# Kernel optimization log

Measured on AMD Instinct MI355X. Metric: run time of the kernel, lower is better.

The kernel has to match this reference:

```python
import jax, jax.numpy as jnp
import numpy as np

B, N, E, D = 4, 4096, 2048, 128
MAX_L = 10


def setup_inputs() -> dict:
    key = jax.random.key(0)
    ks = jax.random.split(key, 8)
    x = jax.random.normal(ks[0], (B, N, D), dtype=jnp.float32)
    incidence = jax.random.uniform(ks[1], (B, N, E), dtype=jnp.float32)
    edge_orders = jax.random.randint(ks[2], (B, E), 0, MAX_L + 1)
    # positive normalizer to avoid division blow-up
    prefix_normalizer = jax.random.uniform(ks[3], (B, E), dtype=jnp.float32) + 0.5
    node_mask = jnp.ones((B, N), dtype=bool)
    edge_mask = jnp.ones((B, E), dtype=bool)
    n_nodes = jnp.full((B,), float(N), dtype=jnp.float32)
    # learned tables: Positional2DWeight(2, max_l+1, D, D) and PositionalWeight(max_l+1, 1, D)
    w_table = jax.random.normal(ks[4], (2, MAX_L + 1, D, D), dtype=jnp.float32) * (1.0 / np.sqrt(D))
    b_table = jax.random.normal(ks[5], (MAX_L + 1, D), dtype=jnp.float32) * 0.02
    return {"x": x, "incidence": incidence, "edge_orders": edge_orders,
            "prefix_normalizer": prefix_normalizer, "node_mask": node_mask,
            "edge_mask": edge_mask, "n_nodes": n_nodes,
            "w_table": w_table, "b_table": b_table}


def reference(x, incidence, edge_orders, prefix_normalizer, node_mask, edge_mask,
              n_nodes, w_table, b_table):
    # mask invalid nodes
    x = jnp.where(node_mask[..., None], x, 0.0)  # [B,N,D]
    # per-edge weight gather (the duplicated [B,E,D,D] tensors)
    w0 = w_table[0][edge_orders]  # [B,E,D,D]
    w1 = w_table[1][edge_orders]  # [B,E,D,D]
    w0_1 = w_table[0, 1]          # [D,D]
    w1_1 = w_table[1, 1]          # [D,D]
    # global mean pooling over nodes
    x0 = jnp.sum(x, axis=1, keepdims=True) / n_nodes[:, None, None]  # [B,1,D]
    # incidence-based V2E aggregation
    x1_e = jnp.einsum('bne,bnd->bed', incidence, x) / prefix_normalizer[..., None]
    x1_e = jnp.where(edge_mask[..., None], x1_e, 0.0)  # [B,E,D]
    # node branch: shared order-1 weights
    x_v = jnp.einsum('bnd,do->bno', x0, w0_1) + jnp.einsum('bnd,do->bno', x, w1_1)
    # edge branch: per-edge-order weights
    x_e = jnp.einsum('bd,bedo->beo', x0[:, 0], w0) + jnp.einsum('bed,bedo->beo', x1_e, w1)
    x_v = jnp.where(node_mask[..., None], x_v, 0.0)
    x_e = jnp.where(edge_mask[..., None], x_e, 0.0)
    # BiasE
    bias_e = b_table[edge_orders]            # [B,E,D]
    bias_1 = b_table[1][None, None, :]       # [1,1,D]
    x_v = jnp.where(node_mask[..., None], x_v + bias_1, 0.0)
    x_e = jnp.where(edge_mask[..., None], x_e + bias_e, 0.0)
    return x_v, x_e
```

## Files before the change

### kernel.cpp

```cpp
#include <hip/hip_runtime.h>

#define Bb 4
#define Nn 4096
#define Ee 2048
#define Dd 128
#define NL 11
#define NTMAX 560
#define ZS 4
#define CH 256
#define NP (CH / 2)
#define LDP 132
#define NCHUNK ((Nn / ZS) / CH)
#define NB_EIN (Bb * (Ee / 32) * ZS)
#define NB_XV (Bb * (Nn / 64))

typedef unsigned short u16;
typedef unsigned int u32;
typedef __attribute__((ext_vector_type(8))) short short8;
typedef __attribute__((ext_vector_type(4))) float floatx4;

__device__ __forceinline__ u32 pk2(float lo, float hi) {
    u32 r;
    asm("v_cvt_pk_bf16_f32 %0, %1, %2" : "=v"(r) : "v"(lo), "v"(hi));
    return r;
}
union S8U { u32 u[4]; short8 s; };

__global__ __launch_bounds__(256) void k_prep(const float* __restrict__ x,
                                              const float* __restrict__ wt,
                                              const int* __restrict__ ord,
                                              u32* __restrict__ xt,
                                              float* __restrict__ part,
                                              u32* __restrict__ wt1T,
                                              int* __restrict__ cnt,
                                              int* __restrict__ offs,
                                              int* __restrict__ idx,
                                              int* __restrict__ tilemap) {
    int blk = blockIdx.x, t = threadIdx.x;
    if (blk < 2048) {
        int b = blk & 3, n0b = (blk >> 2) & 127, d0b = blk >> 9;
        int n0 = n0b * 32, d0 = d0b * 32;
        __shared__ float tile[32][33];
        int r = t >> 5, c = t & 31;
#pragma unroll
        for (int i = 0; i < 4; i++)
            tile[r + 8 * i][c] = x[((size_t)b * Nn + n0 + r + 8 * i) * Dd + d0 + c];
        __syncthreads();
#pragma unroll
        for (int i = 0; i < 2; i++) {
            int idx2 = t + 256 * i;
            int dl = idx2 >> 4, cp = idx2 & 15;
            u32 v = pk2(tile[2 * cp][dl], tile[2 * cp + 1][dl]);
            xt[(size_t)(b * Dd + d0 + dl) * (Nn / 2) + (n0 >> 1) + cp] = v;
        }
        if (t < 32) {
            float s = 0.f;
#pragma unroll
            for (int rr = 0; rr < 32; rr++) s += tile[rr][t];
            part[((size_t)(b * 4 + d0b) * 128 + n0b) * 32 + t] = s;
        }
    } else if (blk < 2224) {
        int rr = blk - 2048;
        int l = rr >> 4, sub = rr & 15;
        int d0 = (sub >> 2) * 32, o0 = (sub & 3) * 32;
        __shared__ float tile[32][33];
        const float* w1 = wt + (size_t)(NL + l) * Dd * Dd;
        int r = t >> 5, c = t & 31;
#pragma unroll
        for (int i = 0; i < 4; i++)
            tile[r + 8 * i][c] = w1[(size_t)(d0 + r + 8 * i) * Dd + o0 + c];
        __syncthreads();
#pragma unroll
        for (int i = 0; i < 2; i++) {
            int idx2 = t + 256 * i;
            int ol = idx2 >> 4, dp = idx2 & 15;
            u32 v = pk2(tile[2 * dp][ol], tile[2 * dp + 1][ol]);
            wt1T[(size_t)(l * Dd + o0 + ol) * (Dd / 2) + (d0 >> 1) + dp] = v;
        }
    } else {
        __shared__ int scnt[Bb * NL], soff[Bb * NL], scur[Bb * NL];
        if (t < Bb * NL) { scnt[t] = 0; scur[t] = 0; }
        __syncthreads();
        for (int g = t; g < Bb * Ee; g += 256)
            atomicAdd(&scnt[(g >> 11) * NL + ord[g]], 1);
        __syncthreads();
        if (t == 0) {
            int off = 0, pos = 0;
            for (int i = 0; i < Bb * NL; i++) {
                soff[i] = off;
                offs[i] = off;
                cnt[i] = scnt[i];
                int al = (scnt[i] + 15) & ~15;
                off += al;
                for (int j = 0; j < (al >> 4); j++) tilemap[pos++] = (i << 16) | j;
            }
            for (; pos < NTMAX; pos++) tilemap[pos] = -1;
        }
        for (int i = t; i < 8960; i += 256) idx[i] = 0;
        __syncthreads();
        for (int g = t; g < Bb * Ee; g += 256) {
            int bk = (g >> 11) * NL + ord[g];
            int pos = soff[bk] + atomicAdd(&scur[bk], 1);
            idx[pos] = g & 2047;
        }
    }
}

__global__ __launch_bounds__(128) void k_xe0(const float* __restrict__ part,
                                             const float* __restrict__ wt,
                                             const float* __restrict__ bt,
                                             float* __restrict__ xe0b) {
    int b = blockIdx.x, l = blockIdx.y, o = threadIdx.x;
    __shared__ float ssum[Dd];
    const float* pp = part + ((size_t)(b * 4 + (o >> 5)) * 128) * 32 + (o & 31);
    float s = 0.f;
    for (int nb = 0; nb < 128; nb++) s += pp[nb * 32];
    ssum[o] = s;
    __syncthreads();
    const float* w0 = wt + (size_t)l * Dd * Dd + o;
    float acc = 0.f;
    for (int d = 0; d < Dd; ++d) acc += ssum[d] * w0[(size_t)d * Dd];
    xe0b[(b * NL + l) * Dd + o] = acc * (1.0f / Nn) + bt[l * Dd + o];
}

__global__ __launch_bounds__(256, 4) void k_main(const float* __restrict__ inc,
                                                 const u32* __restrict__ xt,
                                                 const float* __restrict__ x,
                                                 const u32* __restrict__ wt1T,
                                                 const float* __restrict__ xe0b,
                                                 float* __restrict__ x1p,
                                                 float* __restrict__ outv) {
    int blk = blockIdx.x, t = threadIdx.x;
    int w = t >> 6, lane = t & 63, lm = lane & 15, quad = lane >> 4;
    if (blk < NB_EIN) {
        int b = blk & 3, et0 = ((blk >> 2) & 63) * 32, s = blk >> 8;
        int nbase = s * (Nn / ZS);
        __shared__ u32 bufA[2][32][LDP];
        const float* src = inc + ((size_t)b * Nn + nbase) * Ee + et0;
        int pr = t >> 3, c4 = t & 7;

        const u32* bp0 = xt + ((size_t)b * Dd + w * 32 + lm) * (Nn / 2) + (nbase >> 1);
        const u32* bp1 = bp0 + (size_t)16 * (Nn / 2);
        floatx4 a00 = {0.f,0.f,0.f,0.f}, a01 = {0.f,0.f,0.f,0.f};
        floatx4 a10 = {0.f,0.f,0.f,0.f}, a11 = {0.f,0.f,0.f,0.f};

        float4 sA[8], sB[8];
        auto ldchunk = [&](int ci, float4* st) {
#pragma unroll
            for (int j = 0; j < 4; j++) {
                const float* p0 = src + (size_t)(ci * CH + 2 * (pr + 32 * j)) * Ee + 4 * c4;
                st[2 * j]     = *(const float4*)p0;
                st[2 * j + 1] = *(const float4*)(p0 + Ee);
            }
        };
        auto wrchunk = [&](int cb, const float4* st) {
#pragma unroll
            for (int j = 0; j < 4; j++) {
                bufA[cb][4 * c4 + 0][pr + 32 * j] = pk2(st[2 * j].x, st[2 * j + 1].x);
                bufA[cb][4 * c4 + 1][pr + 32 * j] = pk2(st[2 * j].y, st[2 * j + 1].y);
                bufA[cb][4 * c4 + 2][pr + 32 * j] = pk2(st[2 * j].z, st[2 * j + 1].z);
                bufA[cb][4 * c4 + 3][pr + 32 * j] = pk2(st[2 * j].w, st[2 * j + 1].w);
            }
        };
        ldchunk(0, sA);
        ldchunk(1, sB);
        wrchunk(0, sA);
        __syncthreads();

        for (int i = 0; i < NCHUNK; i++) {
            int cb = i & 1;
            if (i + 2 < NCHUNK) { if (cb == 0) ldchunk(i + 2, sA); else ldchunk(i + 2, sB); }
            int ko = i * NP;
#pragma unroll
            for (int ks = 0; ks < 8; ks++) {
                short8 A0 = *(const short8*)&bufA[cb][lm][ks * 16 + quad * 4];
                short8 A1 = *(const short8*)&bufA[cb][16 + lm][ks * 16 + quad * 4];
                short8 B0 = *(const short8*)(bp0 + ko + ks * 16 + quad * 4);
                short8 B1 = *(const short8*)(bp1 + ko + ks * 16 + quad * 4);
                a00 = __builtin_amdgcn_mfma_f32_16x16x32_bf16(A0, B0, a00, 0, 0, 0);
                a01 = __builtin_amdgcn_mfma_f32_16x16x32_bf16(A0, B1, a01, 0, 0, 0);
                a10 = __builtin_amdgcn_mfma_f32_16x16x32_bf16(A1, B0, a10, 0, 0, 0);
                a11 = __builtin_amdgcn_mfma_f32_16x16x32_bf16(A1, B1, a11, 0, 0, 0);
            }
            if (i < NCHUNK - 1) { if (cb == 0) wrchunk(1, sB); else wrchunk(0, sA); }
            __syncthreads();
        }

        int db = w * 32 + lm;
        float* base = x1p + ((size_t)(s * Bb + b) * Ee) * Dd;
#pragma unroll
        for (int r = 0; r < 4; r++) {
            float* q0 = base + (size_t)(et0 + quad * 4 + r) * Dd;
            q0[db] = a00[r];
            q0[db + 16] = a01[r];
            float* q1 = base + (size_t)(et0 + 16 + quad * 4 + r) * Dd;
            q1[db] = a10[r];
            q1[db + 16] = a11[r];
        }
    } else {
        int rr = blk - NB_EIN;
        int b = rr & 3, n0 = (rr >> 2) * 64;
        const float* xrow = x + ((size_t)b * Nn + n0 + w * 16 + lm) * Dd;
        const u32* wrow = wt1T + (size_t)1 * Dd * (Dd / 2);
        floatx4 acc[8];
#pragma unroll
        for (int ot = 0; ot < 8; ot++) acc[ot] = (floatx4){0.f, 0.f, 0.f, 0.f};
#pragma unroll
        for (int ks = 0; ks < 4; ks++) {
            float4 va = *(const float4*)(xrow + ks * 32 + quad * 8);
            float4 vb = *(const float4*)(xrow + ks * 32 + quad * 8 + 4);
            S8U A;
            A.u[0] = pk2(va.x, va.y); A.u[1] = pk2(va.z, va.w);
            A.u[2] = pk2(vb.x, vb.y); A.u[3] = pk2(vb.z, vb.w);
#pragma unroll
            for (int ot = 0; ot < 8; ot++) {
                short8 Bf = *(const short8*)(wrow + (size_t)(ot * 16 + lm) * (Dd / 2) +
                                             ks * 16 + quad * 4);
                acc[ot] = __builtin_amdgcn_mfma_f32_16x16x32_bf16(A.s, Bf, acc[ot], 0, 0, 0);
            }
        }
#pragma unroll
        for (int ot = 0; ot < 8; ot++) {
            float basev = xe0b[(b * NL + 1) * Dd + ot * 16 + lm];
#pragma unroll
            for (int r = 0; r < 4; r++)
                outv[((size_t)b * Nn + n0 + w * 16 + quad * 4 + r) * Dd + ot * 16 + lm] =
                    acc[ot][r] + basev;
        }
    }
}

__global__ __launch_bounds__(256) void k_epi(const float* __restrict__ x1p,
                                             const float* __restrict__ pref,
                                             const u32* __restrict__ wt1T,
                                             const float* __restrict__ xe0b,
                                             const int* __restrict__ cnt,
                                             const int* __restrict__ offs,
                                             const int* __restrict__ idx,
                                             const int* __restrict__ tilemap,
                                             float* __restrict__ oute) {
    int t = threadIdx.x, w = t >> 6, lane = t & 63, lm = lane & 15, quad = lane >> 4;
    int ent = tilemap[blockIdx.x * 4 + w];
    if (ent < 0) return;
    int bk = ent >> 16, j = ent & 0xffff;
    int bb = bk / NL, l = bk % NL;
    int off = offs[bk], cntv = cnt[bk];
    int eA = idx[off + j * 16 + lm];
    float rp = 1.0f / pref[bb * Ee + eA];
    const float* p0 = x1p + ((size_t)bb * Ee + eA) * Dd;
    const u32* wrow = wt1T + (size_t)l * Dd * (Dd / 2);
    floatx4 acc[8];
#pragma unroll
    for (int ot = 0; ot < 8; ot++) acc[ot] = (floatx4){0.f, 0.f, 0.f, 0.f};
#pragma unroll
    for (int ks = 0; ks < 4; ks++) {
        int d0 = ks * 32 + quad * 8;
        float4 u0 = *(const float4*)(p0 + d0);
        float4 u1 = *(const float4*)(p0 + d0 + 4);
#pragma unroll
        for (int s = 1; s < ZS; s++) {
            const float* ps = p0 + (size_t)s * Bb * Ee * Dd;
            float4 v0 = *(const float4*)(ps + d0);
            float4 v1 = *(const float4*)(ps + d0 + 4);
            u0.x += v0.x; u0.y += v0.y; u0.z += v0.z; u0.w += v0.w;
            u1.x += v1.x; u1.y += v1.y; u1.z += v1.z; u1.w += v1.w;
        }
        S8U A;
        A.u[0] = pk2(u0.x * rp, u0.y * rp);
        A.u[1] = pk2(u0.z * rp, u0.w * rp);
        A.u[2] = pk2(u1.x * rp, u1.y * rp);
        A.u[3] = pk2(u1.z * rp, u1.w * rp);
#pragma unroll
        for (int ot = 0; ot < 8; ot++) {
            short8 Bf = *(const short8*)(wrow + (size_t)(ot * 16 + lm) * (Dd / 2) +
                                         ks * 16 + quad * 4);
            acc[ot] = __builtin_amdgcn_mfma_f32_16x16x32_bf16(A.s, Bf, acc[ot], 0, 0, 0);
        }
    }
    int4 rid = *(const int4*)&idx[off + j * 16 + quad * 4];
    int rowbase = j * 16 + quad * 4;
#pragma unroll
    for (int ot = 0; ot < 8; ot++) {
        float basev = xe0b[(bb * NL + l) * Dd + ot * 16 + lm];
#pragma unroll
        for (int r = 0; r < 4; r++) {
            if (rowbase + r < cntv) {
                int e = ((const int*)&rid)[r];
                oute[((size_t)bb * Ee + e) * Dd + ot * 16 + lm] = acc[ot][r] + basev;
            }
        }
    }
}

extern "C" void kernel_launch(void* const* d_in, const int* in_sizes, int n_in,
                              void* d_out, int out_size, void* d_ws,
                              size_t ws_size, hipStream_t stream) {
    const float* x    = (const float*)d_in[0];
    const float* inc  = (const float*)d_in[1];
    const int*   ord  = (const int*)d_in[2];
    const float* pref = (const float*)d_in[3];
    const float* wt   = (const float*)d_in[7];
    const float* bt   = (const float*)d_in[8];

    float* outv = (float*)d_out;
    float* oute = outv + (size_t)Bb * Nn * Dd;

    float* ws      = (float*)d_ws;
    float* xe0b    = ws + 512;
    int*   cnt     = (int*)(ws + 6144);
    int*   offs    = (int*)(ws + 6192);
    int*   tilemap = (int*)(ws + 6288);
    float* part    = ws + 8192;
    u32*   xt      = (u32*)(ws + 8192 + 65536);
    u32*   wt1T    = (u32*)(ws + 8192 + 65536 + 1048576);
    int*   idx     = (int*)(ws + 8192 + 65536 + 1048576 + 90112);
    float* x1p     = ws + 8192 + 65536 + 1048576 + 90112 + 8960;

    k_prep<<<2225, 256, 0, stream>>>(x, wt, ord, xt, part, wt1T, cnt, offs, idx,
                                     tilemap);
    k_xe0<<<dim3(Bb, NL), 128, 0, stream>>>(part, wt, bt, xe0b);
    k_main<<<NB_EIN + NB_XV, 256, 0, stream>>>(inc, xt, x, wt1T, xe0b, x1p, outv);
    k_epi<<<NTMAX / 4, 256, 0, stream>>>(x1p, pref, wt1T, xe0b, cnt, offs, idx,
                                         tilemap, oute);
}
```

Baseline: 297.4 us.

## Pre-transpose incidence to bf16 in prep kernel; load MFMA operands directly from global

Adds 8192 blocks to the prep kernel that transpose the fp32 incidence tensor into an edge-major, node-pair-packed bf16 buffer in workspace. The V2E MFMA kernel then reads both A and B operands straight from global memory, dropping its LDS double-buffer, the in-loop conversion and the barriers. This moves the layout work out of the GEMM so the GEMM can run at higher occupancy (launch bound minimum of 4 removed). The cost is an extra 64 MB bf16 write plus readback, and the new prep path still reads the full 128 MB fp32 input once.

```diff
diff --git a/kernel.cpp b/kernel.cpp
--- a/kernel.cpp
+++ b/kernel.cpp
@@ -7,12 +7,10 @@
 #define NL 11
 #define NTMAX 560
 #define ZS 4
-#define CH 256
-#define NP (CH / 2)
-#define LDP 132
-#define NCHUNK ((Nn / ZS) / CH)
 #define NB_EIN (Bb * (Ee / 32) * ZS)
 #define NB_XV (Bb * (Nn / 64))
+#define NB_TRX 2048
+#define NB_PACK 8192
 
 typedef unsigned short u16;
 typedef unsigned int u32;
@@ -27,58 +25,80 @@
 union S8U { u32 u[4]; short8 s; };
 
 __global__ __launch_bounds__(256) void k_prep(const float* __restrict__ x,
+                                              const float* __restrict__ inc,
                                               const float* __restrict__ wt,
                                               const int* __restrict__ ord,
                                               u32* __restrict__ xt,
+                                              u32* __restrict__ inct,
                                               float* __restrict__ part,
                                               u32* __restrict__ wt1T,
                                               int* __restrict__ cnt,
                                               int* __restrict__ offs,
                                               int* __restrict__ idx,
                                               int* __restrict__ tilemap) {
+    __shared__ float tP[32][129];
+    __shared__ float tT[32][33];
+    __shared__ int ib[3 * Bb * NL];
     int blk = blockIdx.x, t = threadIdx.x;
-    if (blk < 2048) {
+    if (blk < NB_TRX) {
         int b = blk & 3, n0b = (blk >> 2) & 127, d0b = blk >> 9;
         int n0 = n0b * 32, d0 = d0b * 32;
-        __shared__ float tile[32][33];
         int r = t >> 5, c = t & 31;
 #pragma unroll
         for (int i = 0; i < 4; i++)
-            tile[r + 8 * i][c] = x[((size_t)b * Nn + n0 + r + 8 * i) * Dd + d0 + c];
+            tT[r + 8 * i][c] = x[((size_t)b * Nn + n0 + r + 8 * i) * Dd + d0 + c];
         __syncthreads();
 #pragma unroll
         for (int i = 0; i < 2; i++) {
             int idx2 = t + 256 * i;
             int dl = idx2 >> 4, cp = idx2 & 15;
-            u32 v = pk2(tile[2 * cp][dl], tile[2 * cp + 1][dl]);
+            u32 v = pk2(tT[2 * cp][dl], tT[2 * cp + 1][dl]);
             xt[(size_t)(b * Dd + d0 + dl) * (Nn / 2) + (n0 >> 1) + cp] = v;
         }
         if (t < 32) {
             float s = 0.f;
 #pragma unroll
-            for (int rr = 0; rr < 32; rr++) s += tile[rr][t];
+            for (int rr = 0; rr < 32; rr++) s += tT[rr][t];
             part[((size_t)(b * 4 + d0b) * 128 + n0b) * 32 + t] = s;
         }
-    } else if (blk < 2224) {
-        int rr = blk - 2048;
+    } else if (blk < NB_TRX + NB_PACK) {
+        int rr = blk - NB_TRX;
+        int b = rr & 3, nb = (rr >> 2) & 127, ebg = rr >> 9;
+        int n0 = nb * 32, e0 = ebg * 128;
+        int r = t >> 3, c4 = t & 7;
+        const float* src = inc + ((size_t)b * Nn + n0 + r) * Ee + e0 + c4 * 16;
+#pragma unroll
+        for (int k = 0; k < 4; k++)
+            *(float4*)&tP[r][c4 * 16 + k * 4] = *(const float4*)(src + k * 4);
+        __syncthreads();
+        int ol = t >> 1, half = t & 1;
+        u32* op = inct + (size_t)(b * Ee + e0 + ol) * (Nn / 2) + nb * 16 + half * 8;
+#pragma unroll
+        for (int np = 0; np < 8; np++) {
+            int pair = half * 8 + np;
+            op[np] = pk2(tP[2 * pair][ol], tP[2 * pair + 1][ol]);
+        }
+    } else if (blk < NB_TRX + NB_PACK + 176) {
+        int rr = blk - (NB_TRX + NB_PACK);
         int l = rr >> 4, sub = rr & 15;
         int d0 = (sub >> 2) * 32, o0 = (sub & 3) * 32;
-        __shared__ float tile[32][33];
         const float* w1 = wt + (size_t)(NL + l) * Dd * Dd;
         int r = t >> 5, c = t & 31;
 #pragma unroll
         for (int i = 0; i < 4; i++)
-            tile[r + 8 * i][c] = w1[(size_t)(d0 + r + 8 * i) * Dd + o0 + c];
+            tT[r + 8 * i][c] = w1[(size_t)(d0 + r + 8 * i) * Dd + o0 + c];
         __syncthreads();
 #pragma unroll
         for (int i = 0; i < 2; i++) {
             int idx2 = t + 256 * i;
             int ol = idx2 >> 4, dp = idx2 & 15;
-            u32 v = pk2(tile[2 * dp][ol], tile[2 * dp + 1][ol]);
+            u32 v = pk2(tT[2 * dp][ol], tT[2 * dp + 1][ol]);
             wt1T[(size_t)(l * Dd + o0 + ol) * (Dd / 2) + (d0 >> 1) + dp] = v;
         }
     } else {
-        __shared__ int scnt[Bb * NL], soff[Bb * NL], scur[Bb * NL];
+        int* scnt = ib;
+        int* soff = ib + Bb * NL;
+        int* scur = ib + 2 * Bb * NL;
         if (t < Bb * NL) { scnt[t] = 0; scur[t] = 0; }
         __syncthreads();
         for (int g = t; g < Bb * Ee; g += 256)
@@ -123,69 +143,39 @@
     xe0b[(b * NL + l) * Dd + o] = acc * (1.0f / Nn) + bt[l * Dd + o];
 }
 
-__global__ __launch_bounds__(256, 4) void k_main(const float* __restrict__ inc,
-                                                 const u32* __restrict__ xt,
-                                                 const float* __restrict__ x,
-                                                 const u32* __restrict__ wt1T,
-                                                 const float* __restrict__ xe0b,
-                                                 float* __restrict__ x1p,
-                                                 float* __restrict__ outv) {
+__global__ __launch_bounds__(256) void k_main(const u32* __restrict__ inct,
+                                              const u32* __restrict__ xt,
+                                              const float* __restrict__ x,
+                                              const u32* __restrict__ wt1T,
+                                              const float* __restrict__ xe0b,
+                                              float* __restrict__ x1p,
+                                              float* __restrict__ outv) {
     int blk = blockIdx.x, t = threadIdx.x;
     int w = t >> 6, lane = t & 63, lm = lane & 15, quad = lane >> 4;
     if (blk < NB_EIN) {
         int b = blk & 3, et0 = ((blk >> 2) & 63) * 32, s = blk >> 8;
         int nbase = s * (Nn / ZS);
-        __shared__ u32 bufA[2][32][LDP];
-        const float* src = inc + ((size_t)b * Nn + nbase) * Ee + et0;
-        int pr = t >> 3, c4 = t & 7;
-
-        const u32* bp0 = xt + ((size_t)b * Dd + w * 32 + lm) * (Nn / 2) + (nbase >> 1);
+        const u32* ap0 = inct + (size_t)(b * Ee + et0 + lm) * (Nn / 2) + (nbase >> 1);
+        const u32* ap1 = ap0 + (size_t)16 * (Nn / 2);
+        const u32* bp0 = xt + (size_t)(b * Dd + w * 32 + lm) * (Nn / 2) + (nbase >> 1);
         const u32* bp1 = bp0 + (size_t)16 * (Nn / 2);
         floatx4 a00 = {0.f,0.f,0.f,0.f}, a01 = {0.f,0.f,0.f,0.f};
         floatx4 a10 = {0.f,0.f,0.f,0.f}, a11 = {0.f,0.f,0.f,0.f};
-
-        float4 sA[8], sB[8];
-        auto ldchunk = [&](int ci, float4* st) {
-#pragma unroll
-            for (int j = 0; j < 4; j++) {
-                const float* p0 = src + (size_t)(ci * CH + 2 * (pr + 32 * j)) * Ee + 4 * c4;
-                st[2 * j]     = *(const float4*)p0;
-                st[2 * j + 1] = *(const float4*)(p0 + Ee);
-            }
-        };
-        auto wrchunk = [&](int cb, const float4* st) {
-#pragma unroll
-            for (int j = 0; j < 4; j++) {
-                bufA[cb][4 * c4 + 0][pr + 32 * j] = pk2(st[2 * j].x, st[2 * j + 1].x);
-                bufA[cb][4 * c4 + 1][pr + 32 * j] = pk2(st[2 * j].y, st[2 * j + 1].y);
-                bufA[cb][4 * c4 + 2][pr + 32 * j] = pk2(st[2 * j].z, st[2 * j + 1].z);
-                bufA[cb][4 * c4 + 3][pr + 32 * j] = pk2(st[2 * j].w, st[2 * j + 1].w);
-            }
-        };
-        ldchunk(0, sA);
-        ldchunk(1, sB);
-        wrchunk(0, sA);
-        __syncthreads();
-
-        for (int i = 0; i < NCHUNK; i++) {
-            int cb = i & 1;
-            if (i + 2 < NCHUNK) { if (cb == 0) ldchunk(i + 2, sA); else ldchunk(i + 2, sB); }
-            int ko = i * NP;
+        for (int ci = 0; ci < 4; ci++) {
+            int ko = ci * 128;
 #pragma unroll
             for (int ks = 0; ks < 8; ks++) {
-                short8 A0 = *(const short8*)&bufA[cb][lm][ks * 16 + quad * 4];
-                short8 A1 = *(const short8*)&bufA[cb][16 + lm][ks * 16 + quad * 4];
-                short8 B0 = *(const short8*)(bp0 + ko + ks * 16 + quad * 4);
-                short8 B1 = *(const short8*)(bp1 + ko + ks * 16 + quad * 4);
+                int o = ko + ks * 16 + quad * 4;
+                short8 A0 = *(const short8*)(ap0 + o);
+                short8 A1 = *(const short8*)(ap1 + o);
+                short8 B0 = *(const short8*)(bp0 + o);
+                short8 B1 = *(const short8*)(bp1 + o);
                 a00 = __builtin_amdgcn_mfma_f32_16x16x32_bf16(A0, B0, a00, 0, 0, 0);
                 a01 = __builtin_amdgcn_mfma_f32_16x16x32_bf16(A0, B1, a01, 0, 0, 0);
                 a10 = __builtin_amdgcn_mfma_f32_16x16x32_bf16(A1, B0, a10, 0, 0, 0);
                 a11 = __builtin_amdgcn_mfma_f32_16x16x32_bf16(A1, B1, a11, 0, 0, 0);
             }
-            if (i < NCHUNK - 1) { if (cb == 0) wrchunk(1, sB); else wrchunk(0, sA); }
-            __syncthreads();
-        }
-
+        }
         int db = w * 32 + lm;
         float* base = x1p + ((size_t)(s * Bb + b) * Ee) * Dd;
 #pragma unroll
@@ -315,11 +305,12 @@
     u32*   wt1T    = (u32*)(ws + 8192 + 65536 + 1048576);
     int*   idx     = (int*)(ws + 8192 + 65536 + 1048576 + 90112);
     float* x1p     = ws + 8192 + 65536 + 1048576 + 90112 + 8960;
-
-    k_prep<<<2225, 256, 0, stream>>>(x, wt, ord, xt, part, wt1T, cnt, offs, idx,
-                                     tilemap);
+    u32*   inct    = (u32*)(x1p + (size_t)ZS * Bb * Ee * Dd);
+
+    k_prep<<<NB_TRX + NB_PACK + 176 + 1, 256, 0, stream>>>(
+        x, inc, wt, ord, xt, inct, part, wt1T, cnt, offs, idx, tilemap);
     k_xe0<<<dim3(Bb, NL), 128, 0, stream>>>(part, wt, bt, xe0b);
-    k_main<<<NB_EIN + NB_XV, 256, 0, stream>>>(inc, xt, x, wt1T, xe0b, x1p, outv);
+    k_main<<<NB_EIN + NB_XV, 256, 0, stream>>>(inct, xt, x, wt1T, xe0b, x1p, outv);
     k_epi<<<NTMAX / 4, 256, 0, stream>>>(x1p, pref, wt1T, xe0b, cnt, offs, idx,
                                          tilemap, oute);
 }
```

After: 352.1 us. 1.18x slower.
